# Kernel tuning notes

Hardware: AMD Instinct MI355X
Metric: run time of the kernel (lower is better)

Reference implementation:

```python
import jax, jax.numpy as jnp
import numpy as np

B, T = 32, 2048
STATE, ACT, LAT, ENC = 128, 16, 256, 1024  # input_dim = STATE + 2*ACT = 160


def setup_inputs() -> dict:
    key = jax.random.key(0)
    ks = jax.random.split(key, 16)
    s = lambda k, shp, sc=0.05: jax.random.normal(k, shp, dtype=jnp.float32) * sc
    return {
        "padded_input": jax.random.normal(ks[0], (B, T, STATE + 2 * ACT), dtype=jnp.float32),
        "enc_w1": s(ks[1], (STATE, ENC)), "enc_b1": s(ks[2], (ENC,)),
        "enc_w2": s(ks[3], (ENC, ENC)),   "enc_b2": s(ks[4], (ENC,)),
        "enc_w3": s(ks[5], (ENC, LAT)),   "enc_b3": s(ks[6], (LAT,)),
        "a_diag": jax.random.uniform(ks[7], (LAT,), minval=-0.8, maxval=0.8, dtype=jnp.float32),
        "B_w": s(ks[8], (ACT, LAT)),
        "dec_w1": s(ks[9], (LAT, ENC)),  "dec_b1": s(ks[10], (ENC,)),
        "dec_w2": s(ks[11], (ENC, ENC)), "dec_b2": s(ks[12], (ENC,)),
        "dec_w3": s(ks[13], (ENC, STATE)), "dec_b3": s(ks[14], (STATE,)),
        "nwarmup": 4,
    }


def reference(padded_input, enc_w1, enc_b1, enc_w2, enc_b2, enc_w3, enc_b3,
              a_diag, B_w, dec_w1, dec_b1, dec_w2, dec_b2, dec_w3, dec_b3,
              nwarmup):
    # slice state / actuator channels
    x_t = padded_input[:, :, :STATE]                      # [B,T,STATE]
    u_t1 = padded_input[:, :, STATE + ACT:]               # [B,T,ACT]

    def encoder(x):
        h = jnp.tanh(x @ enc_w1 + enc_b1)
        h = jnp.tanh(h @ enc_w2 + enc_b2)
        return jnp.tanh(h @ enc_w3 + enc_b3)

    def decoder(z):
        h = jnp.tanh(z @ dec_w1 + dec_b1)
        h = jnp.tanh(h @ dec_w2 + dec_b2)
        return h @ dec_w3 + dec_b3

    z_t = encoder(x_t)                                    # [B,T,LAT]
    a = jnp.clip(a_diag, -0.95, 0.95)                     # clamped diagonal of A
    Bu = u_t1 @ B_w                                       # [B,T,LAT]

    # diagonal linear recurrence with warmup resets (reset_probability=0)
    zT = jnp.swapaxes(z_t, 0, 1)                          # [T,B,LAT]
    BuT = jnp.swapaxes(Bu, 0, 1)                          # [T,B,LAT]
    ts = jnp.arange(T)

    def step(prev, inputs):
        z, bu, t = inputs
        inp = jnp.where(t <= nwarmup, z, prev)
        out = a * inp + bu
        return out, out

    _, outs = jax.lax.scan(step, z_t[:, 0, :], (zT, BuT, ts))
    z_t1 = jnp.swapaxes(outs, 0, 1)                       # [B,T,LAT]
    return decoder(z_t1)                                  # [B,T,STATE]
```

## Files before the change

kernel.cpp:

```cpp
#include <hip/hip_runtime.h>
#include <stdint.h>
#include <type_traits>

#define B_ 32
#define T_ 2048
#define STATE_ 128
#define ACT_ 16
#define LAT_ 256
#define ENC_ 1024
#define ROWS_ (B_ * T_)
#define TENC_ 128
#define MENC_ (B_ * TENC_)
#define NCHUNK_ 64
#define LCHUNK_ 32
#define SLAB_ 32768
#define NSLAB_ 2

using bf16x8 = __attribute__((ext_vector_type(8))) short;
using f32x4  = __attribute__((ext_vector_type(4))) float;

__device__ __forceinline__ uint16_t f2bf(float f) {
  uint32_t u = __float_as_uint(f);
  u += 0x7fff + ((u >> 16) & 1);
  return (uint16_t)(u >> 16);
}

__device__ __forceinline__ float fast_tanh(float x) {
  float e = __expf(2.f * x);
  return 1.f - 2.f / (e + 1.f);
}

__device__ __forceinline__ void xcd_remap(int gx, int gy, int& bm, int& bn) {
  if (((gy & 7) == 0) && ((gx & (gx - 1)) == 0)) {
    const int lin  = blockIdx.y * gx + blockIdx.x;
    const int xcd  = lin & 7;
    const int slot = lin >> 3;
    const int lgx  = 31 - __clz(gx);
    bn = slot & (gx - 1);
    bm = ((slot >> lgx) << 3) + xcd;
  } else {
    bm = blockIdx.y;
    bn = blockIdx.x;
  }
}

template <bool TANH, typename OUT_T>
__device__ __forceinline__ void store4(OUT_T* C, size_t m, int N, int nb,
                                       const float* bias, f32x4 a) {
  const float4 bv = *(const float4*)(bias + nb);
  float v0 = a[0] + bv.x, v1 = a[1] + bv.y, v2 = a[2] + bv.z, v3 = a[3] + bv.w;
  if (TANH) {
    v0 = fast_tanh(v0); v1 = fast_tanh(v1);
    v2 = fast_tanh(v2); v3 = fast_tanh(v3);
  }
  if constexpr (std::is_same<OUT_T, uint16_t>::value) {
    uint32_t p0 = (uint32_t)f2bf(v0) | ((uint32_t)f2bf(v1) << 16);
    uint32_t p1 = (uint32_t)f2bf(v2) | ((uint32_t)f2bf(v3) << 16);
    uint2 p = {p0, p1};
    *(uint2*)(C + m * N + nb) = p;
  } else {
    float4 p = {v0, v1, v2, v3};
    *(float4*)(C + m * N + nb) = p;
  }
}

template <bool TANH, typename OUT_T>
__global__ __launch_bounds__(256) void gemm_bt(
    const uint16_t* __restrict__ A, const uint16_t* __restrict__ Bt,
    const float* __restrict__ bias, OUT_T* __restrict__ C,
    int M, int N, int K) {
  __shared__ uint16_t smA[128 * 64];
  __shared__ uint16_t smB[128 * 64];
  const int tid  = threadIdx.x;
  const int lane = tid & 63;
  const int wave = tid >> 6;
  const int wm = wave >> 1, wn = wave & 1;
  const int lr = lane & 15, quad = lane >> 4;

  int bm, bn;
  xcd_remap(gridDim.x, gridDim.y, bm, bn);
  const int m0 = bm * 128;
  const int n0 = bn * 128;

  const int srow = wave * 32 + (lane >> 3);
  const int sblk = lane & 7;

  f32x4 vzero = {0.f, 0.f, 0.f, 0.f};
  f32x4 acc[4][4];
#pragma unroll
  for (int i = 0; i < 4; ++i)
#pragma unroll
    for (int j = 0; j < 4; ++j) acc[i][j] = vzero;

  for (int k0 = 0; k0 < K; k0 += 64) {
#pragma unroll
    for (int i = 0; i < 4; ++i) {
      const int r  = srow + i * 8;
      const int kb = sblk ^ (r & 7);
      const uint16_t* ga = A  + (size_t)(m0 + r) * K + (k0 + kb * 8);
      const uint16_t* gb = Bt + (size_t)(n0 + r) * K + (k0 + kb * 8);
      uint16_t* la = smA + (size_t)(wave * 32 + i * 8) * 64;
      uint16_t* lb = smB + (size_t)(wave * 32 + i * 8) * 64;
      __builtin_amdgcn_global_load_lds(
          (const __attribute__((address_space(1))) void*)ga,
          (__attribute__((address_space(3))) void*)la, 16, 0, 0);
      __builtin_amdgcn_global_load_lds(
          (const __attribute__((address_space(1))) void*)gb,
          (__attribute__((address_space(3))) void*)lb, 16, 0, 0);
    }
    __syncthreads();

#pragma unroll
    for (int ks = 0; ks < 2; ++ks) {
      bf16x8 af[4], bfr[4];
#pragma unroll
      for (int mt = 0; mt < 4; ++mt) {
        const int row  = wm * 64 + mt * 16 + lr;
        const int slot = (ks * 4 + quad) ^ (lr & 7);
        af[mt] = *(const bf16x8*)(smA + row * 64 + slot * 8);
      }
#pragma unroll
      for (int nt = 0; nt < 4; ++nt) {
        const int row  = wn * 64 + nt * 16 + lr;
        const int slot = (ks * 4 + quad) ^ (lr & 7);
        bfr[nt] = *(const bf16x8*)(smB + row * 64 + slot * 8);
      }
#pragma unroll
      for (int mt = 0; mt < 4; ++mt)
#pragma unroll
        for (int nt = 0; nt < 4; ++nt)
          acc[mt][nt] = __builtin_amdgcn_mfma_f32_16x16x32_bf16(
              bfr[nt], af[mt], acc[mt][nt], 0, 0, 0);
    }
    __syncthreads();
  }

#pragma unroll
  for (int mt = 0; mt < 4; ++mt) {
    const size_t m = m0 + wm * 64 + mt * 16 + lr;
#pragma unroll
    for (int nt = 0; nt < 4; ++nt) {
      const int nb = n0 + wn * 64 + nt * 16 + quad * 4;
      store4<TANH>(C, m, N, nb, bias, acc[mt][nt]);
    }
  }
}

template <bool TANH, typename OUT_T>
__global__ __launch_bounds__(256) void gemm64(
    const uint16_t* __restrict__ A, const uint16_t* __restrict__ Bt,
    const float* __restrict__ bias, OUT_T* __restrict__ C,
    int M, int N, int K) {
  __shared__ uint16_t smA[64 * 64];
  __shared__ uint16_t smB[128 * 64];
  const int tid  = threadIdx.x;
  const int lane = tid & 63;
  const int wave = tid >> 6;
  const int wm = wave >> 1, wn = wave & 1;
  const int lr = lane & 15, quad = lane >> 4;

  int bm, bn;
  xcd_remap(gridDim.x, gridDim.y, bm, bn);
  const int m0 = bm * 64;
  const int n0 = bn * 128;

  const int sr8  = lane >> 3;
  const int sblk = lane & 7;

  f32x4 vzero = {0.f, 0.f, 0.f, 0.f};
  f32x4 acc[2][4];
#pragma unroll
  for (int i = 0; i < 2; ++i)
#pragma unroll
    for (int j = 0; j < 4; ++j) acc[i][j] = vzero;

  for (int k0 = 0; k0 < K; k0 += 64) {
#pragma unroll
    for (int i = 0; i < 2; ++i) {
      const int r  = wave * 16 + sr8 + i * 8;
      const int kb = sblk ^ (r & 7);
      const uint16_t* ga = A + (size_t)(m0 + r) * K + (k0 + kb * 8);
      uint16_t* la = smA + (size_t)r * 64;
      __builtin_amdgcn_global_load_lds(
          (const __attribute__((address_space(1))) void*)ga,
          (__attribute__((address_space(3))) void*)la, 16, 0, 0);
    }
#pragma unroll
    for (int i = 0; i < 4; ++i) {
      const int r  = wave * 32 + sr8 + i * 8;
      const int kb = sblk ^ (r & 7);
      const uint16_t* gb = Bt + (size_t)(n0 + r) * K + (k0 + kb * 8);
      uint16_t* lb = smB + (size_t)r * 64;
      __builtin_amdgcn_global_load_lds(
          (const __attribute__((address_space(1))) void*)gb,
          (__attribute__((address_space(3))) void*)lb, 16, 0, 0);
    }
    __syncthreads();

#pragma unroll
    for (int ks = 0; ks < 2; ++ks) {
      bf16x8 af[2], bfr[4];
      const int slotx = (ks * 4 + quad);
#pragma unroll
      for (int mt = 0; mt < 2; ++mt) {
        const int row  = wm * 32 + mt * 16 + lr;
        const int slot = slotx ^ (lr & 7);
        af[mt] = *(const bf16x8*)(smA + row * 64 + slot * 8);
      }
#pragma unroll
      for (int nt = 0; nt < 4; ++nt) {
        const int row  = wn * 64 + nt * 16 + lr;
        const int slot = slotx ^ (lr & 7);
        bfr[nt] = *(const bf16x8*)(smB + row * 64 + slot * 8);
      }
#pragma unroll
      for (int mt = 0; mt < 2; ++mt)
#pragma unroll
        for (int nt = 0; nt < 4; ++nt)
          acc[mt][nt] = __builtin_amdgcn_mfma_f32_16x16x32_bf16(
              bfr[nt], af[mt], acc[mt][nt], 0, 0, 0);
    }
    __syncthreads();
  }

#pragma unroll
  for (int mt = 0; mt < 2; ++mt) {
    const size_t m = m0 + wm * 32 + mt * 16 + lr;
#pragma unroll
    for (int nt = 0; nt < 4; ++nt) {
      const int nb = n0 + wn * 64 + nt * 16 + quad * 4;
      store4<TANH>(C, m, N, nb, bias, acc[mt][nt]);
    }
  }
}

struct TArgs {
  const float* s[6];
  uint16_t* d[6];
  int R[6];
  int C[6];
};

__global__ __launch_bounds__(256) void transpose_cast(TArgs a) {
  __shared__ float tile[32][33];
  const int z = blockIdx.z;
  const float* s = a.s[z];
  uint16_t* d = a.d[z];
  const int R = a.R[z], C = a.C[z];
  const int bc = blockIdx.x * 32, br = blockIdx.y * 32;
  if (bc >= C || br >= R) return;
  const int tx = threadIdx.x & 31, ty = threadIdx.x >> 5;
#pragma unroll
  for (int i = 0; i < 32; i += 8)
    tile[ty + i][tx] = s[(size_t)(br + ty + i) * C + (bc + tx)];
  __syncthreads();
#pragma unroll
  for (int i = 0; i < 32; i += 8)
    d[(size_t)(bc + ty + i) * R + (br + tx)] = f2bf(tile[tx][ty + i]);
}

__global__ __launch_bounds__(256) void cast_x(const float* __restrict__ pin,
                                              uint16_t* __restrict__ Xc) {
  const int idx = blockIdx.x * 256 + threadIdx.x;
  const int r = idx >> 7, c = idx & 127;
  const int b = r >> 7, t = r & 127;
  Xc[idx] = f2bf(pin[((size_t)b * T_ + t) * 160 + c]);
}

__device__ __forceinline__ float clip_a(const float* a_diag, int l) {
  return fminf(fmaxf(a_diag[l], -0.95f), 0.95f);
}

__device__ __forceinline__ float bu_at(const float* __restrict__ pin, int b,
                                       int t, const float* bw) {
  const float* u = pin + ((size_t)b * T_ + t) * 160 + 144;
  float bu = 0.f;
#pragma unroll
  for (int k = 0; k < ACT_; ++k) bu += u[k] * bw[k];
  return bu;
}

__global__ __launch_bounds__(256) void rec_pass1(
    const float* __restrict__ Zc, const float* __restrict__ pin,
    const float* __restrict__ Bw, const float* __restrict__ a_diag,
    const int* __restrict__ nwp, float* __restrict__ F) {
  const int l = threadIdx.x, c = blockIdx.x, b = blockIdx.y;
  const int nw = *nwp;
  const float a = clip_a(a_diag, l);
  float bw[ACT_];
#pragma unroll
  for (int k = 0; k < ACT_; ++k) bw[k] = Bw[k * LAT_ + l];

  float s = (c == 0) ? Zc[(size_t)b * TENC_ * LAT_ + l] : 0.f;
  const int t0 = c * LCHUNK_;
  for (int j = 0; j < LCHUNK_; ++j) {
    const int t = t0 + j;
    float inp;
    if (t <= nw) {
      const int tt = t < TENC_ ? t : TENC_ - 1;
      inp = Zc[((size_t)b * TENC_ + tt) * LAT_ + l];
    } else {
      inp = s;
    }
    s = a * inp + bu_at(pin, b, t, bw);
  }
  F[((size_t)c * B_ + b) * LAT_ + l] = s;
}

__global__ __launch_bounds__(256) void rec_pass2(
    const float* __restrict__ Zc, const float* __restrict__ F,
    const float* __restrict__ a_diag, const int* __restrict__ nwp,
    float* __restrict__ I) {
  const int l = threadIdx.x, b = blockIdx.x;
  const int nw = *nwp;
  const float a = clip_a(a_diag, l);
  float aL = a;
#pragma unroll
  for (int i = 0; i < 5; ++i) aL *= aL;
  float s = Zc[(size_t)b * TENC_ * LAT_ + l];
  I[(size_t)b * LAT_ + l] = s;
  for (int c = 1; c < NCHUNK_; ++c) {
    const float Fp = F[((size_t)(c - 1) * B_ + b) * LAT_ + l];
    const bool exact = ((c - 1) == 0) || (nw >= (c - 1) * LCHUNK_);
    s = exact ? Fp : (aL * s + Fp);
    I[((size_t)c * B_ + b) * LAT_ + l] = s;
  }
}

__global__ __launch_bounds__(256) void rec_pass3(
    const float* __restrict__ Zc, const float* __restrict__ pin,
    const float* __restrict__ Bw, const float* __restrict__ a_diag,
    const int* __restrict__ nwp, const float* __restrict__ I,
    uint16_t* __restrict__ Zp) {
  const int l = threadIdx.x, c = blockIdx.x, b = blockIdx.y;
  const int nw = *nwp;
  const float a = clip_a(a_diag, l);
  float bw[ACT_];
#pragma unroll
  for (int k = 0; k < ACT_; ++k) bw[k] = Bw[k * LAT_ + l];

  float s = I[((size_t)c * B_ + b) * LAT_ + l];
  const int t0 = c * LCHUNK_;
  for (int j = 0; j < LCHUNK_; ++j) {
    const int t = t0 + j;
    float inp;
    if (t <= nw) {
      const int tt = t < TENC_ ? t : TENC_ - 1;
      inp = Zc[((size_t)b * TENC_ + tt) * LAT_ + l];
    } else {
      inp = s;
    }
    s = a * inp + bu_at(pin, b, t, bw);
    Zp[((size_t)b * T_ + t) * LAT_ + l] = f2bf(s);
  }
}

extern "C" void kernel_launch(void* const* d_in, const int* in_sizes, int n_in,
                              void* d_out, int out_size, void* d_ws,
                              size_t ws_size, hipStream_t stream) {
  const float* pin = (const float*)d_in[0];
  const float* ew1 = (const float*)d_in[1];
  const float* eb1 = (const float*)d_in[2];
  const float* ew2 = (const float*)d_in[3];
  const float* eb2 = (const float*)d_in[4];
  const float* ew3 = (const float*)d_in[5];
  const float* eb3 = (const float*)d_in[6];
  const float* adg = (const float*)d_in[7];
  const float* Bw  = (const float*)d_in[8];
  const float* dw1 = (const float*)d_in[9];
  const float* db1 = (const float*)d_in[10];
  const float* dw2 = (const float*)d_in[11];
  const float* db2 = (const float*)d_in[12];
  const float* dw3 = (const float*)d_in[13];
  const float* db3 = (const float*)d_in[14];
  const int* nwp   = (const int*)d_in[15];
  float* out = (float*)d_out;

  uint8_t* ws = (uint8_t*)d_ws;
  size_t off = 0;
  auto alloc = [&](size_t b) -> void* {
    void* p = ws + off;
    off += (b + 255) & ~(size_t)255;
    return p;
  };
  uint16_t* W1t = (uint16_t*)alloc((size_t)ENC_ * STATE_ * 2);
  uint16_t* W2t = (uint16_t*)alloc((size_t)ENC_ * ENC_ * 2);
  uint16_t* W3t = (uint16_t*)alloc((size_t)LAT_ * ENC_ * 2);
  uint16_t* D1t = (uint16_t*)alloc((size_t)ENC_ * LAT_ * 2);
  uint16_t* D2t = (uint16_t*)alloc((size_t)ENC_ * ENC_ * 2);
  uint16_t* D3t = (uint16_t*)alloc((size_t)STATE_ * ENC_ * 2);
  uint16_t* Xc  = (uint16_t*)alloc((size_t)MENC_ * STATE_ * 2);
  float* Zc = (float*)alloc((size_t)MENC_ * LAT_ * 4);
  float* F  = (float*)alloc((size_t)NCHUNK_ * B_ * LAT_ * 4);
  float* I  = (float*)alloc((size_t)NCHUNK_ * B_ * LAT_ * 4);
  uint16_t* Zp = (uint16_t*)alloc((size_t)ROWS_ * LAT_ * 2);
  uint16_t* G1 = (uint16_t*)alloc((size_t)SLAB_ * ENC_ * 2);
  uint16_t* G2 = (uint16_t*)alloc((size_t)SLAB_ * ENC_ * 2);
  uint16_t* H1c = G1;
  uint16_t* H2c = G1 + (size_t)MENC_ * ENC_;

  if (ws_size < off) return;

  TArgs ta;
  ta.s[0] = ew1; ta.d[0] = W1t; ta.R[0] = STATE_; ta.C[0] = ENC_;
  ta.s[1] = ew2; ta.d[1] = W2t; ta.R[1] = ENC_;   ta.C[1] = ENC_;
  ta.s[2] = ew3; ta.d[2] = W3t; ta.R[2] = ENC_;   ta.C[2] = LAT_;
  ta.s[3] = dw1; ta.d[3] = D1t; ta.R[3] = LAT_;   ta.C[3] = ENC_;
  ta.s[4] = dw2; ta.d[4] = D2t; ta.R[4] = ENC_;   ta.C[4] = ENC_;
  ta.s[5] = dw3; ta.d[5] = D3t; ta.R[5] = ENC_;   ta.C[5] = STATE_;
  transpose_cast<<<dim3(32, 32, 6), 256, 0, stream>>>(ta);

  cast_x<<<dim3((MENC_ * STATE_) / 256), 256, 0, stream>>>(pin, Xc);

  gemm_bt<true, uint16_t><<<dim3(ENC_ / 128, MENC_ / 128), 256, 0, stream>>>(
      Xc, W1t, eb1, H1c, MENC_, ENC_, STATE_);
  gemm_bt<true, uint16_t><<<dim3(ENC_ / 128, MENC_ / 128), 256, 0, stream>>>(
      H1c, W2t, eb2, H2c, MENC_, ENC_, ENC_);
  gemm64<true, float><<<dim3(LAT_ / 128, MENC_ / 64), 256, 0, stream>>>(
      H2c, W3t, eb3, Zc, MENC_, LAT_, ENC_);

  rec_pass1<<<dim3(NCHUNK_, B_), 256, 0, stream>>>(Zc, pin, Bw, adg, nwp, F);
  rec_pass2<<<dim3(B_), 256, 0, stream>>>(Zc, F, adg, nwp, I);
  rec_pass3<<<dim3(NCHUNK_, B_), 256, 0, stream>>>(Zc, pin, Bw, adg, nwp, I,
                                                   Zp);

  for (int s = 0; s < NSLAB_; ++s) {
    const uint16_t* Zs = Zp + (size_t)s * SLAB_ * LAT_;
    float* Os = out + (size_t)s * SLAB_ * STATE_;
    gemm_bt<true, uint16_t><<<dim3(ENC_ / 128, SLAB_ / 128), 256, 0, stream>>>(
        Zs, D1t, db1, G1, SLAB_, ENC_, LAT_);
    gemm_bt<true, uint16_t><<<dim3(ENC_ / 128, SLAB_ / 128), 256, 0, stream>>>(
        G1, D2t, db2, G2, SLAB_, ENC_, ENC_);
    gemm64<false, float><<<dim3(STATE_ / 128, SLAB_ / 64), 256, 0, stream>>>(
        G2, D3t, db3, Os, SLAB_, STATE_, ENC_);
  }
}
```

Before: 535.4 us.

## Use 32x32x16 MFMA in main GEMM and run decoder as one slab when workspace allows

The 128x128 GEMM kernel now uses 32x32x16 bf16 MFMA tiles (2x2 per wave) in place of 16x16x32 tiles (4x4 per wave). This cuts LDS fragment loads per MFMA and raises work per instruction. Separately, the decoder runs over all rows in a single slab when the workspace is large enough, halving its launch count and enlarging the grids. The single-slab path needs more workspace and falls back to two slabs otherwise. The new accumulator layout also changes the epilogue store pattern.

```diff
diff --git a/kernel.cpp b/kernel.cpp
--- a/kernel.cpp
+++ b/kernel.cpp
@@ -14,10 +14,10 @@
 #define NCHUNK_ 64
 #define LCHUNK_ 32
 #define SLAB_ 32768
-#define NSLAB_ 2
 
 using bf16x8 = __attribute__((ext_vector_type(8))) short;
 using f32x4  = __attribute__((ext_vector_type(4))) float;
+using f32x16 = __attribute__((ext_vector_type(16))) float;
 
 __device__ __forceinline__ uint16_t f2bf(float f) {
   uint32_t u = __float_as_uint(f);
@@ -75,7 +75,7 @@
   const int lane = tid & 63;
   const int wave = tid >> 6;
   const int wm = wave >> 1, wn = wave & 1;
-  const int lr = lane & 15, quad = lane >> 4;
+  const int l32 = lane & 31, h = lane >> 5;
 
   int bm, bn;
   xcd_remap(gridDim.x, gridDim.y, bm, bn);
@@ -85,12 +85,13 @@
   const int srow = wave * 32 + (lane >> 3);
   const int sblk = lane & 7;
 
-  f32x4 vzero = {0.f, 0.f, 0.f, 0.f};
-  f32x4 acc[4][4];
-#pragma unroll
-  for (int i = 0; i < 4; ++i)
-#pragma unroll
-    for (int j = 0; j < 4; ++j) acc[i][j] = vzero;
+  f32x16 acc[2][2];
+#pragma unroll
+  for (int i = 0; i < 2; ++i)
+#pragma unroll
+    for (int j = 0; j < 2; ++j)
+#pragma unroll
+      for (int r = 0; r < 16; ++r) acc[i][j][r] = 0.f;
 
   for (int k0 = 0; k0 < K; k0 += 64) {
 #pragma unroll
@@ -111,37 +112,43 @@
     __syncthreads();
 
 #pragma unroll
-    for (int ks = 0; ks < 2; ++ks) {
-      bf16x8 af[4], bfr[4];
-#pragma unroll
-      for (int mt = 0; mt < 4; ++mt) {
-        const int row  = wm * 64 + mt * 16 + lr;
-        const int slot = (ks * 4 + quad) ^ (lr & 7);
+    for (int ks = 0; ks < 4; ++ks) {
+      bf16x8 af[2], bfr[2];
+      const int kslot = ks * 2 + h;
+#pragma unroll
+      for (int mt = 0; mt < 2; ++mt) {
+        const int row  = wm * 64 + mt * 32 + l32;
+        const int slot = kslot ^ (row & 7);
         af[mt] = *(const bf16x8*)(smA + row * 64 + slot * 8);
       }
 #pragma unroll
-      for (int nt = 0; nt < 4; ++nt) {
-        const int row  = wn * 64 + nt * 16 + lr;
-        const int slot = (ks * 4 + quad) ^ (lr & 7);
+      for (int nt = 0; nt < 2; ++nt) {
+        const int row  = wn * 64 + nt * 32 + l32;
+        const int slot = kslot ^ (row & 7);
         bfr[nt] = *(const bf16x8*)(smB + row * 64 + slot * 8);
       }
 #pragma unroll
-      for (int mt = 0; mt < 4; ++mt)
-#pragma unroll
-        for (int nt = 0; nt < 4; ++nt)
-          acc[mt][nt] = __builtin_amdgcn_mfma_f32_16x16x32_bf16(
+      for (int mt = 0; mt < 2; ++mt)
+#pragma unroll
+        for (int nt = 0; nt < 2; ++nt)
+          acc[mt][nt] = __builtin_amdgcn_mfma_f32_32x32x16_bf16(
               bfr[nt], af[mt], acc[mt][nt], 0, 0, 0);
     }
     __syncthreads();
   }
 
 #pragma unroll
-  for (int mt = 0; mt < 4; ++mt) {
-    const size_t m = m0 + wm * 64 + mt * 16 + lr;
-#pragma unroll
-    for (int nt = 0; nt < 4; ++nt) {
-      const int nb = n0 + wn * 64 + nt * 16 + quad * 4;
-      store4<TANH>(C, m, N, nb, bias, acc[mt][nt]);
+  for (int mt = 0; mt < 2; ++mt) {
+    const size_t m = m0 + wm * 64 + mt * 32 + l32;
+#pragma unroll
+    for (int nt = 0; nt < 2; ++nt) {
+#pragma unroll
+      for (int q = 0; q < 4; ++q) {
+        const int nb = n0 + wn * 64 + nt * 32 + q * 8 + h * 4;
+        f32x4 v = {acc[mt][nt][4 * q + 0], acc[mt][nt][4 * q + 1],
+                   acc[mt][nt][4 * q + 2], acc[mt][nt][4 * q + 3]};
+        store4<TANH>(C, m, N, nb, bias, v);
+      }
     }
   }
 }
@@ -394,8 +401,16 @@
   float* F  = (float*)alloc((size_t)NCHUNK_ * B_ * LAT_ * 4);
   float* I  = (float*)alloc((size_t)NCHUNK_ * B_ * LAT_ * 4);
   uint16_t* Zp = (uint16_t*)alloc((size_t)ROWS_ * LAT_ * 2);
-  uint16_t* G1 = (uint16_t*)alloc((size_t)SLAB_ * ENC_ * 2);
-  uint16_t* G2 = (uint16_t*)alloc((size_t)SLAB_ * ENC_ * 2);
+
+  const size_t full_g = (size_t)ROWS_ * ENC_ * 2;
+  int slab_rows, nslab;
+  if (ws_size >= off + 2 * (full_g + 256)) {
+    slab_rows = ROWS_;  nslab = 1;
+  } else {
+    slab_rows = SLAB_;  nslab = 2;
+  }
+  uint16_t* G1 = (uint16_t*)alloc((size_t)slab_rows * ENC_ * 2);
+  uint16_t* G2 = (uint16_t*)alloc((size_t)slab_rows * ENC_ * 2);
   uint16_t* H1c = G1;
   uint16_t* H2c = G1 + (size_t)MENC_ * ENC_;
 
@@ -424,14 +439,17 @@
   rec_pass3<<<dim3(NCHUNK_, B_), 256, 0, stream>>>(Zc, pin, Bw, adg, nwp, I,
                                                    Zp);
 
-  for (int s = 0; s < NSLAB_; ++s) {
-    const uint16_t* Zs = Zp + (size_t)s * SLAB_ * LAT_;
-    float* Os = out + (size_t)s * SLAB_ * STATE_;
-    gemm_bt<true, uint16_t><<<dim3(ENC_ / 128, SLAB_ / 128), 256, 0, stream>>>(
-        Zs, D1t, db1, G1, SLAB_, ENC_, LAT_);
-    gemm_bt<true, uint16_t><<<dim3(ENC_ / 128, SLAB_ / 128), 256, 0, stream>>>(
-        G1, D2t, db2, G2, SLAB_, ENC_, ENC_);
-    gemm64<false, float><<<dim3(STATE_ / 128, SLAB_ / 64), 256, 0, stream>>>(
-        G2, D3t, db3, Os, SLAB_, STATE_, ENC_);
-  }
-}
+  for (int s = 0; s < nslab; ++s) {
+    const uint16_t* Zs = Zp + (size_t)s * slab_rows * LAT_;
+    float* Os = out + (size_t)s * slab_rows * STATE_;
+    gemm_bt<true, uint16_t><<<dim3(ENC_ / 128, slab_rows / 128), 256, 0,
+                              stream>>>(Zs, D1t, db1, G1, slab_rows, ENC_,
+                                        LAT_);
+    gemm_bt<true, uint16_t><<<dim3(ENC_ / 128, slab_rows / 128), 256, 0,
+                              stream>>>(G1, D2t, db2, G2, slab_rows, ENC_,
+                                        ENC_);
+    gemm64<false, float><<<dim3(STATE_ / 128, slab_rows / 64), 256, 0,
+                           stream>>>(G2, D3t, db3, Os, slab_rows, STATE_,
+                                     ENC_);
+  }
+}
```

After: 520.7 us. 1.03x faster.
